# Kernel tuning notes

Hardware: AMD Instinct MI355X
Metric: run time of the kernel (lower is better)

Reference implementation:

```python
import jax, jax.numpy as jnp
import numpy as np

N_NODES = 100000

def gcn_conv(x, W, b, src, dst, n_nodes):
    # PyG GCNConv: out = D^{-1/2} (A + I) D^{-1/2} (x W) + b, deg includes self-loop
    h = x @ W  # [N, H]
    ones = jnp.ones(src.shape[0], dtype=x.dtype)
    deg = jax.ops.segment_sum(ones, dst, num_segments=n_nodes) + 1.0  # +1 self-loop
    dinv = jax.lax.rsqrt(deg)  # deg >= 1, no zeros
    norm = dinv[src] * dinv[dst]  # [E]
    msg = h[src] * norm[:, None]  # [E, H] gather + scale
    agg = jax.ops.segment_sum(msg, dst, num_segments=n_nodes)  # scatter-add
    self_contrib = h * (dinv * dinv)[:, None]  # self-loop term norm = dinv_i^2
    return agg + self_contrib + b


def setup_inputs() -> dict:
    key = jax.random.key(0)
    ks = jax.random.split(key, 6)
    F_IN, H, E = 128, 128, 1600000
    x = jax.random.normal(ks[0], (N_NODES, F_IN), dtype=jnp.float32)
    edge_index = jax.random.randint(ks[1], (2, E), 0, N_NODES, dtype=jnp.int32)
    s = 1.0 / np.sqrt(F_IN)
    W1 = jax.random.normal(ks[2], (F_IN, H), dtype=jnp.float32) * s
    b1 = jnp.zeros((H,), dtype=jnp.float32)
    W2 = jax.random.normal(ks[3], (H, H), dtype=jnp.float32) * (1.0 / np.sqrt(H))
    b2 = jnp.zeros((H,), dtype=jnp.float32)
    Wlin = jax.random.normal(ks[4], (H, 1), dtype=jnp.float32) * (1.0 / np.sqrt(H))
    blin = jnp.zeros((1,), dtype=jnp.float32)
    return {"x": x, "edge_index": edge_index, "W1": W1, "b1": b1,
            "W2": W2, "b2": b2, "Wlin": Wlin, "blin": blin}


def reference(x, edge_index, W1, b1, W2, b2, Wlin, blin):
    src, dst = edge_index[0], edge_index[1]
    h = gcn_conv(x, W1, b1, src, dst, N_NODES)
    h = jax.nn.relu(h)
    h = gcn_conv(h, W2, b2, src, dst, N_NODES)
    h = jax.nn.relu(h)
    out = h @ Wlin + blin  # [N, 1]
    return out.squeeze(-1)  # [N]
```

## Files before the change

### kernel.cpp

```cpp
#include <hip/hip_runtime.h>
#include <hip/hip_fp16.h>

#define NFEAT 128

typedef _Float16 v8hf __attribute__((ext_vector_type(8)));
typedef float v4f __attribute__((ext_vector_type(4)));

__global__ void k_deg_rank(const int* __restrict__ dst, int* __restrict__ deg,
                           int* __restrict__ rank, int E) {
  int e = blockIdx.x * blockDim.x + threadIdx.x;
  if (e < E) rank[e] = atomicAdd(&deg[dst[e]], 1);
}

__global__ void k_fill(int* __restrict__ p, int v, int n) {
  int i = blockIdx.x * 256 + threadIdx.x;
  if (i < n) p[i] = v;
}

__global__ void k_prep_w(const float* __restrict__ W1, const float* __restrict__ W2,
                         _Float16* __restrict__ Wt1, _Float16* __restrict__ Wt2) {
  int idx = blockIdx.x * 256 + threadIdx.x;
  const float* W = (idx < 16384) ? W1 : W2;
  _Float16* Wt = (idx < 16384) ? Wt1 : Wt2;
  int i = idx & 16383;
  int k = i >> 7, n = i & 127;
  Wt[n * 128 + k] = (_Float16)W[k * 128 + n];
}

__global__ __launch_bounds__(1024) void k_scan_blocks(const int* __restrict__ deg,
    int* __restrict__ base, int* __restrict__ partials, int n) {
  __shared__ int buf[1024];
  int tid = threadIdx.x;
  int i = blockIdx.x * 1024 + tid;
  int v = (i < n) ? ((deg[i] + 7) & ~7) : 0;
  buf[tid] = v;
  __syncthreads();
  #pragma unroll
  for (int off = 1; off < 1024; off <<= 1) {
    int t = (tid >= off) ? buf[tid - off] : 0;
    __syncthreads();
    buf[tid] += t;
    __syncthreads();
  }
  if (i <= n) base[i] = buf[tid] - v;
  if (tid == 1023) partials[blockIdx.x] = buf[tid];
}

__global__ void k_scan_partials(int* __restrict__ partials, int nb) {
  __shared__ int buf[128];
  int tid = threadIdx.x;
  int v = (tid < nb) ? partials[tid] : 0;
  buf[tid] = v;
  __syncthreads();
  #pragma unroll
  for (int off = 1; off < 128; off <<= 1) {
    int t = (tid >= off) ? buf[tid - off] : 0;
    __syncthreads();
    buf[tid] += t;
    __syncthreads();
  }
  if (tid < nb) partials[tid] = buf[tid] - v;
}

__global__ void k_finalize_base(int* __restrict__ base, const int* __restrict__ partials,
    const int* __restrict__ deg, float* __restrict__ dinv, int n) {
  int i = blockIdx.x * blockDim.x + threadIdx.x;
  if (i <= n) {
    base[i] += partials[i >> 10];
    if (i < n) dinv[i] = rsqrtf((float)(deg[i] + 1));
  }
}

__global__ void k_scatter(const int* __restrict__ src, const int* __restrict__ dst,
    const int* __restrict__ rank, const int* __restrict__ base,
    int* __restrict__ ssrc, int E) {
  int e = blockIdx.x * blockDim.x + threadIdx.x;
  if (e < E) ssrc[base[dst[e]] + rank[e]] = src[e];
}

__global__ void k_zero_row(_Float16* __restrict__ g16, int N) {
  int i = threadIdx.x;
  int s = i >> 4, m = i & 15;
  g16[((size_t)s * (N + 1) + N) * 16 + m] = (_Float16)0.f;
}

template <typename AT>
__global__ __launch_bounds__(256) void k_gemm_mfma(
    const AT* __restrict__ A, const _Float16* __restrict__ Wt,
    const float* __restrict__ dinv, _Float16* __restrict__ g16, int N) {
  __shared__ _Float16 As[64][136];
  __shared__ _Float16 Ws[128][136];
  const int tid = threadIdx.x;
  const int row0 = blockIdx.x * 64;

  if constexpr (sizeof(AT) == 4) {
    #pragma unroll
    for (int i = 0; i < 8; i++) {
      int idx = tid + i * 256;
      int row = idx >> 5;
      int c4 = idx & 31;
      int gr = row0 + row; gr = (gr < N) ? gr : (N - 1);
      float4 v = *(const float4*)((const float*)A + (size_t)gr * NFEAT + c4 * 4);
      _Float16* p = &As[row][c4 * 4];
      p[0] = (_Float16)v.x; p[1] = (_Float16)v.y;
      p[2] = (_Float16)v.z; p[3] = (_Float16)v.w;
    }
  } else {
    #pragma unroll
    for (int i = 0; i < 4; i++) {
      int idx = tid + i * 256;
      int row = idx >> 4;
      int c8 = idx & 15;
      int gr = row0 + row; gr = (gr < N) ? gr : (N - 1);
      *(uint4*)&As[row][c8 * 8] =
          *(const uint4*)((const _Float16*)A + (size_t)gr * NFEAT + c8 * 8);
    }
  }
  #pragma unroll
  for (int i = 0; i < 8; i++) {
    int idx = tid + i * 256;
    int row = idx >> 4;
    int c8 = idx & 15;
    *(uint4*)&Ws[row][c8 * 8] = *(const uint4*)(Wt + (size_t)row * 128 + c8 * 8);
  }
  __syncthreads();

  const int wv = tid >> 6;
  const int lane = tid & 63;
  const int m = lane & 15;
  const int q = lane >> 4;

  v4f acc[8] = {};
  const _Float16* arow = &As[wv * 16 + m][0];
  #pragma unroll
  for (int kt = 0; kt < 4; kt++) {
    v8hf af = *(const v8hf*)(arow + kt * 32 + q * 8);
    #pragma unroll
    for (int ct = 0; ct < 8; ct++) {
      v8hf bf = *(const v8hf*)(&Ws[ct * 16 + m][kt * 32 + q * 8]);
      acc[ct] = __builtin_amdgcn_mfma_f32_16x16x32_f16(af, bf, acc[ct], 0, 0, 0);
    }
  }

  int nd[4]; float dv[4];
  #pragma unroll
  for (int r = 0; r < 4; r++) {
    nd[r] = row0 + wv * 16 + q * 4 + r;
    int c = (nd[r] < N) ? nd[r] : (N - 1);
    dv[r] = dinv[c];
  }
  #pragma unroll
  for (int ct = 0; ct < 8; ct++)
    #pragma unroll
    for (int r = 0; r < 4; r++)
      if (nd[r] < N)
        g16[((size_t)ct * (N + 1) + nd[r]) * 16 + m] = (_Float16)(acc[ct][r] * dv[r]);
}

__global__ __launch_bounds__(256) void k_agg_slice(
    const __half2* __restrict__ g16, const float* __restrict__ dinv,
    const int* __restrict__ base, const int* __restrict__ ssrc,
    const float* __restrict__ bias, __half2* __restrict__ hB, int N) {
  const int lane = threadIdx.x & 63;
  const int wv = threadIdx.x >> 6;
  const int s = blockIdx.x & 7;
  const int p = lane >> 3, d = lane & 7;
  const int n = (blockIdx.x >> 3) * 32 + wv * 8 + p;
  const bool act = (n < N);
  const int nc = act ? n : (N - 1);
  const __half2* table = g16 + (size_t)s * (N + 1) * 8;

  float2 a0 = __half22float2(table[(size_t)nc * 8 + d]);
  float2 a1 = make_float2(0.f, 0.f);
  int e = base[nc], b1e = base[nc + 1];
  if (!act) b1e = e;
  for (; e < b1e; e += 8) {
    int4 ia = *(const int4*)(ssrc + e);
    int4 ib = *(const int4*)(ssrc + e + 4);
    float2 f0 = __half22float2(table[(size_t)ia.x * 8 + d]);
    float2 f1 = __half22float2(table[(size_t)ia.y * 8 + d]);
    float2 f2 = __half22float2(table[(size_t)ia.z * 8 + d]);
    float2 f3 = __half22float2(table[(size_t)ia.w * 8 + d]);
    float2 f4 = __half22float2(table[(size_t)ib.x * 8 + d]);
    float2 f5 = __half22float2(table[(size_t)ib.y * 8 + d]);
    float2 f6 = __half22float2(table[(size_t)ib.z * 8 + d]);
    float2 f7 = __half22float2(table[(size_t)ib.w * 8 + d]);
    a0.x += (f0.x + f1.x) + (f2.x + f3.x);
    a0.y += (f0.y + f1.y) + (f2.y + f3.y);
    a1.x += (f4.x + f5.x) + (f6.x + f7.x);
    a1.y += (f4.y + f5.y) + (f6.y + f7.y);
  }
  if (act) {
    float dvn = dinv[n];
    float2 bb = *(const float2*)(bias + s * 16 + d * 2);
    hB[(size_t)n * 64 + s * 8 + d] =
        __floats2half2_rn(fmaxf((a0.x + a1.x) * dvn + bb.x, 0.f),
                          fmaxf((a0.y + a1.y) * dvn + bb.y, 0.f));
  }
}

__global__ __launch_bounds__(256) void k_agg_final_slice(
    const __half2* __restrict__ g16, const float* __restrict__ dinv,
    const int* __restrict__ base, const int* __restrict__ ssrc,
    const float* __restrict__ bias, const float* __restrict__ wlin,
    const float* __restrict__ blin, float* __restrict__ out, int N) {
  const int lane = threadIdx.x & 63;
  const int wv = threadIdx.x >> 6;
  const int s = blockIdx.x & 7;
  const int p = lane >> 3, d = lane & 7;
  const int n = (blockIdx.x >> 3) * 32 + wv * 8 + p;
  const bool act = (n < N);
  const int nc = act ? n : (N - 1);
  const __half2* table = g16 + (size_t)s * (N + 1) * 8;

  float2 a0 = __half22float2(table[(size_t)nc * 8 + d]);
  float2 a1 = make_float2(0.f, 0.f);
  int e = base[nc], b1e = base[nc + 1];
  if (!act) b1e = e;
  for (; e < b1e; e += 8) {
    int4 ia = *(const int4*)(ssrc + e);
    int4 ib = *(const int4*)(ssrc + e + 4);
    float2 f0 = __half22float2(table[(size_t)ia.x * 8 + d]);
    float2 f1 = __half22float2(table[(size_t)ia.y * 8 + d]);
    float2 f2 = __half22float2(table[(size_t)ia.z * 8 + d]);
    float2 f3 = __half22float2(table[(size_t)ia.w * 8 + d]);
    float2 f4 = __half22float2(table[(size_t)ib.x * 8 + d]);
    float2 f5 = __half22float2(table[(size_t)ib.y * 8 + d]);
    float2 f6 = __half22float2(table[(size_t)ib.z * 8 + d]);
    float2 f7 = __half22float2(table[(size_t)ib.w * 8 + d]);
    a0.x += (f0.x + f1.x) + (f2.x + f3.x);
    a0.y += (f0.y + f1.y) + (f2.y + f3.y);
    a1.x += (f4.x + f5.x) + (f6.x + f7.x);
    a1.y += (f4.y + f5.y) + (f6.y + f7.y);
  }
  if (act) {
    float dvn = dinv[n];
    float2 bb = *(const float2*)(bias + s * 16 + d * 2);
    float2 wl = *(const float2*)(wlin + s * 16 + d * 2);
    float pv = fmaxf((a0.x + a1.x) * dvn + bb.x, 0.f) * wl.x +
               fmaxf((a0.y + a1.y) * dvn + bb.y, 0.f) * wl.y;
    #pragma unroll
    for (int m = 1; m <= 4; m <<= 1) pv += __shfl_xor(pv, m, 64);
    if (d == 0) atomicAdd(out + n, pv + (s == 0 ? blin[0] : 0.f));
  }
}

extern "C" void kernel_launch(void* const* d_in, const int* in_sizes, int n_in,
                              void* d_out, int out_size, void* d_ws, size_t ws_size,
                              hipStream_t stream) {
  const float* x    = (const float*)d_in[0];
  const int*   ei   = (const int*)d_in[1];
  const float* W1   = (const float*)d_in[2];
  const float* b1   = (const float*)d_in[3];
  const float* W2   = (const float*)d_in[4];
  const float* b2   = (const float*)d_in[5];
  const float* Wlin = (const float*)d_in[6];
  const float* blin = (const float*)d_in[7];
  const int N = in_sizes[0] / NFEAT;
  const int E = in_sizes[1] / 2;
  const int* src = ei;
  const int* dst = ei + E;
  const int Epad = E + 8 * N + 8;

  int* ws_i = (int*)d_ws;
  size_t off = 0;
  int* deg      = ws_i + off; off += N;
  int* base     = ws_i + off; off += (size_t)N + 1;
  off = (off + 3) & ~(size_t)3;
  int* partials = ws_i + off; off += 128;
  int* ssrc     = ws_i + off; off += Epad;
  float* dinv   = (float*)(ws_i + off); off += N;
  off = (off + 3) & ~(size_t)3;
  _Float16* Wt1 = (_Float16*)(ws_i + off); off += 8192;
  _Float16* Wt2 = (_Float16*)(ws_i + off); off += 8192;
  _Float16* g16 = (_Float16*)(ws_i + off); off += (size_t)(N + 1) * 64 + 32;
  _Float16* hB  = (_Float16*)(ws_i + off); off += (size_t)N * 64;
  int* rank     = (int*)g16;

  hipMemsetAsync(deg, 0, (size_t)N * sizeof(int), stream);
  hipMemsetAsync(d_out, 0, (size_t)N * sizeof(float), stream);

  const int tpbE = 256;
  const int gE = (E + tpbE - 1) / tpbE;
  k_deg_rank<<<gE, tpbE, 0, stream>>>(dst, deg, rank, E);
  k_fill<<<(Epad + 255) / 256, 256, 0, stream>>>(ssrc, N, Epad);
  k_prep_w<<<128, 256, 0, stream>>>(W1, W2, Wt1, Wt2);

  const int nb = (N + 1 + 1023) / 1024;
  k_scan_blocks<<<nb, 1024, 0, stream>>>(deg, base, partials, N);
  k_scan_partials<<<1, 128, 0, stream>>>(partials, nb);
  k_finalize_base<<<((N + 1) + 255) / 256, 256, 0, stream>>>(base, partials, deg, dinv, N);
  k_scatter<<<gE, tpbE, 0, stream>>>(src, dst, rank, base, ssrc, E);
  k_zero_row<<<1, 128, 0, stream>>>(g16, N);

  const int gg = (N + 63) / 64;
  const int ga = 8 * ((N + 31) / 32);
  k_gemm_mfma<float><<<gg, 256, 0, stream>>>(x, Wt1, dinv, g16, N);
  k_agg_slice<<<ga, 256, 0, stream>>>((const __half2*)g16, dinv, base, ssrc, b1,
                                      (__half2*)hB, N);
  k_gemm_mfma<_Float16><<<gg, 256, 0, stream>>>(hB, Wt2, dinv, g16, N);
  k_agg_final_slice<<<ga, 256, 0, stream>>>((const __half2*)g16, dinv, base, ssrc, b2,
                                            Wlin, blin, (float*)d_out, N);
}
```

Before: 426.2 us.

## Fold self-loops into CSR and gather 16-byte rows per lane in aggregation

Self-loop edges are now inserted into the CSR, so the degree count already includes them and the separate self-term load goes away. Each node's row padding shrinks from a multiple of 8 to a multiple of 4, which cuts wasted padded gathers. The aggregation kernels now load a full 16-byte half-precision row segment per lane from 4 edge slots in parallel, then combine partial sums with shuffles. The cost is extra shuffle reductions and more registers per lane, traded for wider loads and fewer padded edges.

Result: no change. 429.6 us (+0.8%).

```diff
diff --git a/kernel.cpp b/kernel.cpp
--- a/kernel.cpp
+++ b/kernel.cpp
@@ -7,9 +7,10 @@
 typedef float v4f __attribute__((ext_vector_type(4)));
 
 __global__ void k_deg_rank(const int* __restrict__ dst, int* __restrict__ deg,
-                           int* __restrict__ rank, int E) {
+                           int* __restrict__ rank, int E, int N) {
   int e = blockIdx.x * blockDim.x + threadIdx.x;
   if (e < E) rank[e] = atomicAdd(&deg[dst[e]], 1);
+  else if (e < E + N) rank[e] = atomicAdd(&deg[e - E], 1);
 }
 
 __global__ void k_fill(int* __restrict__ p, int v, int n) {
@@ -32,7 +33,7 @@
   __shared__ int buf[1024];
   int tid = threadIdx.x;
   int i = blockIdx.x * 1024 + tid;
-  int v = (i < n) ? ((deg[i] + 7) & ~7) : 0;
+  int v = (i < n) ? ((deg[i] + 3) & ~3) : 0;
   buf[tid] = v;
   __syncthreads();
   #pragma unroll
@@ -67,15 +68,16 @@
   int i = blockIdx.x * blockDim.x + threadIdx.x;
   if (i <= n) {
     base[i] += partials[i >> 10];
-    if (i < n) dinv[i] = rsqrtf((float)(deg[i] + 1));
+    if (i < n) dinv[i] = rsqrtf((float)deg[i]);
   }
 }
 
 __global__ void k_scatter(const int* __restrict__ src, const int* __restrict__ dst,
     const int* __restrict__ rank, const int* __restrict__ base,
-    int* __restrict__ ssrc, int E) {
+    int* __restrict__ ssrc, int E, int N) {
   int e = blockIdx.x * blockDim.x + threadIdx.x;
   if (e < E) ssrc[base[dst[e]] + rank[e]] = src[e];
+  else if (e < E + N) { int n = e - E; ssrc[base[n] + rank[e]] = n; }
 }
 
 __global__ void k_zero_row(_Float16* __restrict__ g16, int N) {
@@ -158,91 +160,121 @@
 }
 
 __global__ __launch_bounds__(256) void k_agg_slice(
-    const __half2* __restrict__ g16, const float* __restrict__ dinv,
+    const _Float16* __restrict__ g16, const float* __restrict__ dinv,
     const int* __restrict__ base, const int* __restrict__ ssrc,
-    const float* __restrict__ bias, __half2* __restrict__ hB, int N) {
+    const float* __restrict__ bias, _Float16* __restrict__ hB, int N) {
   const int lane = threadIdx.x & 63;
   const int wv = threadIdx.x >> 6;
   const int s = blockIdx.x & 7;
-  const int p = lane >> 3, d = lane & 7;
+  const int p = lane >> 3;
+  const int h = lane & 7;
+  const int part = h & 1;
+  const int slot = h >> 1;
   const int n = (blockIdx.x >> 3) * 32 + wv * 8 + p;
   const bool act = (n < N);
   const int nc = act ? n : (N - 1);
-  const __half2* table = g16 + (size_t)s * (N + 1) * 8;
-
-  float2 a0 = __half22float2(table[(size_t)nc * 8 + d]);
-  float2 a1 = make_float2(0.f, 0.f);
-  int e = base[nc], b1e = base[nc + 1];
-  if (!act) b1e = e;
-  for (; e < b1e; e += 8) {
-    int4 ia = *(const int4*)(ssrc + e);
-    int4 ib = *(const int4*)(ssrc + e + 4);
-    float2 f0 = __half22float2(table[(size_t)ia.x * 8 + d]);
-    float2 f1 = __half22float2(table[(size_t)ia.y * 8 + d]);
-    float2 f2 = __half22float2(table[(size_t)ia.z * 8 + d]);
-    float2 f3 = __half22float2(table[(size_t)ia.w * 8 + d]);
-    float2 f4 = __half22float2(table[(size_t)ib.x * 8 + d]);
-    float2 f5 = __half22float2(table[(size_t)ib.y * 8 + d]);
-    float2 f6 = __half22float2(table[(size_t)ib.z * 8 + d]);
-    float2 f7 = __half22float2(table[(size_t)ib.w * 8 + d]);
-    a0.x += (f0.x + f1.x) + (f2.x + f3.x);
-    a0.y += (f0.y + f1.y) + (f2.y + f3.y);
-    a1.x += (f4.x + f5.x) + (f6.x + f7.x);
-    a1.y += (f4.y + f5.y) + (f6.y + f7.y);
-  }
-  if (act) {
+  const _Float16* table = g16 + (size_t)s * (N + 1) * 16 + part * 8;
+
+  float acc0[8] = {}, acc1[8] = {};
+  int e = base[nc], e1 = base[nc + 1];
+  if (!act) e1 = e;
+  for (; e + 8 <= e1; e += 8) {
+    int2 ii = *(const int2*)(ssrc + e + slot * 2);
+    v8hf r0 = *(const v8hf*)(table + (size_t)ii.x * 16);
+    v8hf r1 = *(const v8hf*)(table + (size_t)ii.y * 16);
+    #pragma unroll
+    for (int j = 0; j < 8; j++) { acc0[j] += (float)r0[j]; acc1[j] += (float)r1[j]; }
+  }
+  if (e < e1) {
+    int si = ssrc[e + slot];
+    v8hf r0 = *(const v8hf*)(table + (size_t)si * 16);
+    #pragma unroll
+    for (int j = 0; j < 8; j++) acc0[j] += (float)r0[j];
+  }
+  float red[8];
+  #pragma unroll
+  for (int j = 0; j < 8; j++) {
+    float v = acc0[j] + acc1[j];
+    v += __shfl_xor(v, 2, 64);
+    v += __shfl_xor(v, 4, 64);
+    red[j] = v;
+  }
+  if (act && slot == 0) {
     float dvn = dinv[n];
-    float2 bb = *(const float2*)(bias + s * 16 + d * 2);
-    hB[(size_t)n * 64 + s * 8 + d] =
-        __floats2half2_rn(fmaxf((a0.x + a1.x) * dvn + bb.x, 0.f),
-                          fmaxf((a0.y + a1.y) * dvn + bb.y, 0.f));
+    const float* bp = bias + s * 16 + part * 8;
+    float4 bb0 = *(const float4*)(bp);
+    float4 bb1 = *(const float4*)(bp + 4);
+    v8hf o;
+    o[0] = (_Float16)fmaxf(red[0] * dvn + bb0.x, 0.f);
+    o[1] = (_Float16)fmaxf(red[1] * dvn + bb0.y, 0.f);
+    o[2] = (_Float16)fmaxf(red[2] * dvn + bb0.z, 0.f);
+    o[3] = (_Float16)fmaxf(red[3] * dvn + bb0.w, 0.f);
+    o[4] = (_Float16)fmaxf(red[4] * dvn + bb1.x, 0.f);
+    o[5] = (_Float16)fmaxf(red[5] * dvn + bb1.y, 0.f);
+    o[6] = (_Float16)fmaxf(red[6] * dvn + bb1.z, 0.f);
+    o[7] = (_Float16)fmaxf(red[7] * dvn + bb1.w, 0.f);
+    *(v8hf*)(hB + (size_t)n * NFEAT + s * 16 + part * 8) = o;
   }
 }
 
 __global__ __launch_bounds__(256) void k_agg_final_slice(
-    const __half2* __restrict__ g16, const float* __restrict__ dinv,
+    const _Float16* __restrict__ g16, const float* __restrict__ dinv,
     const int* __restrict__ base, const int* __restrict__ ssrc,
     const float* __restrict__ bias, const float* __restrict__ wlin,
     const float* __restrict__ blin, float* __restrict__ out, int N) {
   const int lane = threadIdx.x & 63;
   const int wv = threadIdx.x >> 6;
   const int s = blockIdx.x & 7;
-  const int p = lane >> 3, d = lane & 7;
+  const int p = lane >> 3;
+  const int h = lane & 7;
+  const int part = h & 1;
+  const int slot = h >> 1;
   const int n = (blockIdx.x >> 3) * 32 + wv * 8 + p;
   const bool act = (n < N);
   const int nc = act ? n : (N - 1);
-  const __half2* table = g16 + (size_t)s * (N + 1) * 8;
-
-  float2 a0 = __half22float2(table[(size_t)nc * 8 + d]);
-  float2 a1 = make_float2(0.f, 0.f);
-  int e = base[nc], b1e = base[nc + 1];
-  if (!act) b1e = e;
-  for (; e < b1e; e += 8) {
-    int4 ia = *(const int4*)(ssrc + e);
-    int4 ib = *(const int4*)(ssrc + e + 4);
-    float2 f0 = __half22float2(table[(size_t)ia.x * 8 + d]);
-    float2 f1 = __half22float2(table[(size_t)ia.y * 8 + d]);
-    float2 f2 = __half22float2(table[(size_t)ia.z * 8 + d]);
-    float2 f3 = __half22float2(table[(size_t)ia.w * 8 + d]);
-    float2 f4 = __half22float2(table[(size_t)ib.x * 8 + d]);
-    float2 f5 = __half22float2(table[(size_t)ib.y * 8 + d]);
-    float2 f6 = __half22float2(table[(size_t)ib.z * 8 + d]);
-    float2 f7 = __half22float2(table[(size_t)ib.w * 8 + d]);
-    a0.x += (f0.x + f1.x) + (f2.x + f3.x);
-    a0.y += (f0.y + f1.y) + (f2.y + f3.y);
-    a1.x += (f4.x + f5.x) + (f6.x + f7.x);
-    a1.y += (f4.y + f5.y) + (f6.y + f7.y);
-  }
-  if (act) {
-    float dvn = dinv[n];
-    float2 bb = *(const float2*)(bias + s * 16 + d * 2);
-    float2 wl = *(const float2*)(wlin + s * 16 + d * 2);
-    float pv = fmaxf((a0.x + a1.x) * dvn + bb.x, 0.f) * wl.x +
-               fmaxf((a0.y + a1.y) * dvn + bb.y, 0.f) * wl.y;
-    #pragma unroll
-    for (int m = 1; m <= 4; m <<= 1) pv += __shfl_xor(pv, m, 64);
-    if (d == 0) atomicAdd(out + n, pv + (s == 0 ? blin[0] : 0.f));
-  }
+  const _Float16* table = g16 + (size_t)s * (N + 1) * 16 + part * 8;
+
+  float acc0[8] = {}, acc1[8] = {};
+  int e = base[nc], e1 = base[nc + 1];
+  if (!act) e1 = e;
+  for (; e + 8 <= e1; e += 8) {
+    int2 ii = *(const int2*)(ssrc + e + slot * 2);
+    v8hf r0 = *(const v8hf*)(table + (size_t)ii.x * 16);
+    v8hf r1 = *(const v8hf*)(table + (size_t)ii.y * 16);
+    #pragma unroll
+    for (int j = 0; j < 8; j++) { acc0[j] += (float)r0[j]; acc1[j] += (float)r1[j]; }
+  }
+  if (e < e1) {
+    int si = ssrc[e + slot];
+    v8hf r0 = *(const v8hf*)(table + (size_t)si * 16);
+    #pragma unroll
+    for (int j = 0; j < 8; j++) acc0[j] += (float)r0[j];
+  }
+  float red[8];
+  #pragma unroll
+  for (int j = 0; j < 8; j++) {
+    float v = acc0[j] + acc1[j];
+    v += __shfl_xor(v, 2, 64);
+    v += __shfl_xor(v, 4, 64);
+    red[j] = v;
+  }
+  float dvn = dinv[nc];
+  const float* bp = bias + s * 16 + part * 8;
+  const float* wp = wlin + s * 16 + part * 8;
+  float4 bb0 = *(const float4*)(bp);
+  float4 bb1 = *(const float4*)(bp + 4);
+  float4 wl0 = *(const float4*)(wp);
+  float4 wl1 = *(const float4*)(wp + 4);
+  float pv = fmaxf(red[0] * dvn + bb0.x, 0.f) * wl0.x +
+             fmaxf(red[1] * dvn + bb0.y, 0.f) * wl0.y +
+             fmaxf(red[2] * dvn + bb0.z, 0.f) * wl0.z +
+             fmaxf(red[3] * dvn + bb0.w, 0.f) * wl0.w +
+             fmaxf(red[4] * dvn + bb1.x, 0.f) * wl1.x +
+             fmaxf(red[5] * dvn + bb1.y, 0.f) * wl1.y +
+             fmaxf(red[6] * dvn + bb1.z, 0.f) * wl1.z +
+             fmaxf(red[7] * dvn + bb1.w, 0.f) * wl1.w;
+  pv += __shfl_xor(pv, 1, 64);
+  if (act && h == 0) atomicAdd(out + n, pv + (s == 0 ? blin[0] : 0.f));
 }
 
 extern "C" void kernel_launch(void* const* d_in, const int* in_sizes, int n_in,
@@ -260,7 +292,7 @@
   const int E = in_sizes[1] / 2;
   const int* src = ei;
   const int* dst = ei + E;
-  const int Epad = E + 8 * N + 8;
+  const int Epad = E + 5 * N + 8;
 
   int* ws_i = (int*)d_ws;
   size_t off = 0;
@@ -281,8 +313,8 @@
   hipMemsetAsync(d_out, 0, (size_t)N * sizeof(float), stream);
 
   const int tpbE = 256;
-  const int gE = (E + tpbE - 1) / tpbE;
-  k_deg_rank<<<gE, tpbE, 0, stream>>>(dst, deg, rank, E);
+  const int gE = (E + N + tpbE - 1) / tpbE;
+  k_deg_rank<<<gE, tpbE, 0, stream>>>(dst, deg, rank, E, N);
   k_fill<<<(Epad + 255) / 256, 256, 0, stream>>>(ssrc, N, Epad);
   k_prep_w<<<128, 256, 0, stream>>>(W1, W2, Wt1, Wt2);
 
@@ -290,15 +322,14 @@
   k_scan_blocks<<<nb, 1024, 0, stream>>>(deg, base, partials, N);
   k_scan_partials<<<1, 128, 0, stream>>>(partials, nb);
   k_finalize_base<<<((N + 1) + 255) / 256, 256, 0, stream>>>(base, partials, deg, dinv, N);
-  k_scatter<<<gE, tpbE, 0, stream>>>(src, dst, rank, base, ssrc, E);
+  k_scatter<<<gE, tpbE, 0, stream>>>(src, dst, rank, base, ssrc, E, N);
   k_zero_row<<<1, 128, 0, stream>>>(g16, N);
 
   const int gg = (N + 63) / 64;
   const int ga = 8 * ((N + 31) / 32);
   k_gemm_mfma<float><<<gg, 256, 0, stream>>>(x, Wt1, dinv, g16, N);
-  k_agg_slice<<<ga, 256, 0, stream>>>((const __half2*)g16, dinv, base, ssrc, b1,
-                                      (__half2*)hB, N);
+  k_agg_slice<<<ga, 256, 0, stream>>>(g16, dinv, base, ssrc, b1, hB, N);
   k_gemm_mfma<_Float16><<<gg, 256, 0, stream>>>(hB, Wt2, dinv, g16, N);
-  k_agg_final_slice<<<ga, 256, 0, stream>>>((const __half2*)g16, dinv, base, ssrc, b2,
+  k_agg_final_slice<<<ga, 256, 0, stream>>>(g16, dinv, base, ssrc, b2,
                                             Wlin, blin, (float*)d_out, N);
 }
```
